# Performance work log

Hardware: AMD Instinct MI355X
Metric: run time of the kernel (lower is better)

## Reference

```python
import jax, jax.numpy as jnp
import numpy as np

H = 16  # attention heads


def setup_inputs() -> dict:
    key = jax.random.key(0)
    k0, k1, k2 = jax.random.split(key, 3)
    B, T, C = 2, 2048, 1024
    x = jax.random.normal(k0, (B, T, C), dtype=jnp.float32)
    W_attn = jax.random.normal(k1, (3 * C, C), dtype=jnp.float32) * 0.02
    W_proj = jax.random.normal(k2, (C, C), dtype=jnp.float32) * 0.02
    b_proj = jnp.zeros((C,), dtype=jnp.float32)
    return {"x": x, "W_attn": W_attn, "W_proj": W_proj, "b_proj": b_proj}


def reference(x, W_attn, W_proj, b_proj):
    # Eval-mode (dropout = identity), rotational_embeddings=False, flash=False path.
    B, T, C = x.shape
    d = C // H
    qkv = jnp.einsum('btc,fc->btf', x, W_attn)          # [B,T,3C] fused QKV proj
    q, k, v = jnp.split(qkv, 3, axis=-1)
    # [B,T,C] -> [B,H,T,d]
    q = q.reshape(B, T, H, d).transpose(0, 2, 1, 3)
    k = k.reshape(B, T, H, d).transpose(0, 2, 1, 3)
    v = v.reshape(B, T, H, d).transpose(0, 2, 1, 3)
    scale = 1.0 / np.sqrt(d).astype(np.float32)
    att = jnp.einsum('bhqd,bhkd->bhqk', q, k) * scale    # full TxT scores (no mask)
    att = jax.nn.softmax(att, axis=-1)
    y = jnp.einsum('bhqk,bhkd->bhqd', att, v)            # [B,H,T,d]
    y = y.transpose(0, 2, 1, 3).reshape(B, T, C)
    return jnp.einsum('btc,oc->bto', y, W_proj) + b_proj
```

## Files before the change

kernel.cpp:

```cpp
#include <hip/hip_runtime.h>
#include <hip/hip_bf16.h>
#include <stdint.h>

typedef __attribute__((ext_vector_type(8))) short bf16x8;
typedef __attribute__((ext_vector_type(4))) float f32x4;
typedef __attribute__((ext_vector_type(4))) unsigned u32x4;

#define MFMA16(A,B,C) __builtin_amdgcn_mfma_f32_16x16x32_bf16(A,B,C,0,0,0)


__device__ inline void gld_lds16(const __hip_bfloat16* g, __hip_bfloat16* l) {
  __builtin_amdgcn_global_load_lds(
      (const __attribute__((address_space(1))) void*)g,
      (__attribute__((address_space(3))) void*)l, 16, 0, 0);
}

__device__ inline unsigned pkbf(float a, float b) {
  __hip_bfloat162 t = __float22bfloat162_rn(float2{a, b});
  return *(unsigned*)&t;
}

__device__ inline void quad_mix(unsigned &a, unsigned &b) {
#if __has_builtin(__builtin_amdgcn_permlane32_swap) && __has_builtin(__builtin_amdgcn_permlane16_swap)
  auto r1 = __builtin_amdgcn_permlane32_swap(a, b, false, false);
  auto r2 = __builtin_amdgcn_permlane16_swap(r1[0], r1[1], false, false);
  a = r2[0];
  b = r2[1];
#else
  int lane = (int)(threadIdx.x & 63);
  int g = lane >> 4;
  int lm = lane & 15;
  int slo = (((g << 1) & 3) << 4) | lm;
  int shi = ((((g << 1) | 1) & 3) << 4) | lm;
  unsigned t0 = (unsigned)__shfl((int)a, slo, 64);
  unsigned t1 = (unsigned)__shfl((int)b, slo, 64);
  unsigned t2 = (unsigned)__shfl((int)a, shi, 64);
  unsigned t3 = (unsigned)__shfl((int)b, shi, 64);
  bool hi = g >= 2;
  unsigned na = hi ? t1 : t0;
  unsigned nb = hi ? t3 : t2;
  a = na;
  b = nb;
#endif
}

__global__ __launch_bounds__(256)
void cvt_bf16(const float* __restrict__ s0, __hip_bfloat16* __restrict__ d0, int n0,
              const float* __restrict__ s1, __hip_bfloat16* __restrict__ d1, int n1,
              const float* __restrict__ s2, __hip_bfloat16* __restrict__ d2, int n2)
{
  const float* s; __hip_bfloat16* d; int n;
  if      (blockIdx.y == 0) { s = s0; d = d0; n = n0; }
  else if (blockIdx.y == 1) { s = s1; d = d1; n = n1; }
  else                      { s = s2; d = d2; n = n2; }
  int idx = (blockIdx.x * 256 + threadIdx.x) * 8;
  if (idx >= n) return;
  float4 u0 = *(const float4*)(s + idx);
  float4 u1 = *(const float4*)(s + idx + 4);
  __hip_bfloat16 t[8];
  t[0] = __float2bfloat16(u0.x); t[1] = __float2bfloat16(u0.y);
  t[2] = __float2bfloat16(u0.z); t[3] = __float2bfloat16(u0.w);
  t[4] = __float2bfloat16(u1.x); t[5] = __float2bfloat16(u1.y);
  t[6] = __float2bfloat16(u1.z); t[7] = __float2bfloat16(u1.w);
  *(int4*)(d + idx) = *(const int4*)t;
}

template<int BM, int BN, typename TC, bool VT, bool FUSE>
__global__ __launch_bounds__(256)
void gemm_bt(const __hip_bfloat16* __restrict__ A,
             const __hip_bfloat16* __restrict__ B,
             TC* __restrict__ C,
             const float* __restrict__ bias,
             __hip_bfloat16* __restrict__ vtg,
             const float* __restrict__ pl,
             int M, int N, int K)
{
  constexpr int MI = BM / 32;
  constexpr int NJ = BN / 32;
  constexpr int NP = (BM + BN) / 64;
  constexpr int SMEM_E = VT ? (((BM + BN) * 32 > 4 * 64 * 72) ? (BM + BN) * 32
                                                              : 4 * 64 * 72)
                            : (BM + BN) * 32;
  __shared__ __align__(16) __hip_bfloat16 smem[SMEM_E];
  __hip_bfloat16* As = smem;
  __hip_bfloat16* Bs = smem + BM * 32;

  const int tid  = threadIdx.x;
  const int lane = tid & 63;
  const int w    = tid >> 6;
  const int lm   = lane & 15;
  const int g    = lane >> 4;

  const int bm = blockIdx.y * BM;
  const int bn = blockIdx.x * BN;
  const int rm = (w >> 1) * (BM / 2);
  const int cn = (w & 1) * (BN / 2);

  const f32x4 fzero = {0.0f, 0.0f, 0.0f, 0.0f};
  f32x4 acc[MI][NJ];
  for (int i = 0; i < MI; i++)
    for (int j = 0; j < NJ; j++)
      acc[i][j] = fzero;

  for (int k0 = 0; k0 < K; k0 += 32) {
    __syncthreads();
#pragma unroll
    for (int p = 0; p < NP; p++) {
      int c = tid + p * 256;
      if (c < BM * 4) {
        if constexpr (FUSE) {
          int row = bm + (c >> 2);
          int col = k0 + (c & 3) * 8;
          int hh  = col >> 6;
          float li = pl[row * 16 + hh] + pl[(size_t)M * 16 + row * 16 + hh];
          float rinv = 1.0f / li;
          int4 ra = *(const int4*)&A[(size_t)row * K + col];
          int4 rb = *(const int4*)&A[(size_t)M * K + (size_t)row * K + col];
          const __hip_bfloat16* pa = (const __hip_bfloat16*)&ra;
          const __hip_bfloat16* pb = (const __hip_bfloat16*)&rb;
          __hip_bfloat16 tt[8];
#pragma unroll
          for (int jj = 0; jj < 8; jj++)
            tt[jj] = __float2bfloat16(
                (__bfloat162float(pa[jj]) + __bfloat162float(pb[jj])) * rinv);
          *(int4*)&As[c * 8] = *(const int4*)tt;
        } else {
          gld_lds16(&A[(size_t)(bm + (c >> 2)) * K + k0 + (c & 3) * 8],
                    &As[c * 8]);
        }
      } else {
        int cb = c - BM * 4;
        gld_lds16(&B[(size_t)(bn + (cb >> 2)) * K + k0 + (cb & 3) * 8], &Bs[cb * 8]);
      }
    }
    __syncthreads();

    bf16x8 af[MI], bfr[NJ];
#pragma unroll
    for (int i = 0; i < MI; i++)
      af[i] = *(const bf16x8*)&As[(rm + 16 * i + lm) * 32 + 8 * g];
#pragma unroll
    for (int j = 0; j < NJ; j++)
      bfr[j] = *(const bf16x8*)&Bs[(cn + 16 * j + lm) * 32 + 8 * g];
#pragma unroll
    for (int i = 0; i < MI; i++)
#pragma unroll
      for (int j = 0; j < NJ; j++)
        acc[i][j] = MFMA16(af[i], bfr[j], acc[i][j]);
  }

  if constexpr (VT) {
    if (vtg != nullptr && bn >= 2048) {
      __syncthreads();
      __hip_bfloat16* scr = smem + w * (64 * 72);
      const int h  = (bn + cn - 2048) >> 6;
      const int bb = bm >> 11;
      const int t0 = (bm & 2047) + rm;
#pragma unroll
      for (int j = 0; j < NJ; j++) {
        int dd = 16 * j + lm;
#pragma unroll
        for (int i = 0; i < MI; i++) {
          __hip_bfloat16 t4[4];
#pragma unroll
          for (int r = 0; r < 4; r++) t4[r] = __float2bfloat16(acc[i][j][r]);
          *(int2*)&scr[dd * 72 + 16 * i + 4 * g] = *(const int2*)t4;
        }
      }
      asm volatile("s_waitcnt lgkmcnt(0)" ::: "memory");
      const int u = lane & 7, ddl = lane >> 3;
#pragma unroll
      for (int it = 0; it < 8; it++) {
        int dd = it * 8 + ddl;
        int4 vrow = *(const int4*)&scr[dd * 72 + u * 8];
        *(int4*)&vtg[((size_t)(bb * 16 + h) * 64 + dd) * 2048 + t0 + u * 8] =
            vrow;
      }
      return;
    }
  }

  const float qs = (VT && vtg != nullptr && bn < 1024)
                       ? (0.125f * 1.4426950408889634f) : 1.0f;
#pragma unroll
  for (int j = 0; j < NJ; j++) {
    int coln = bn + cn + 16 * j + lm;
    float bv = bias ? bias[coln] : 0.0f;
#pragma unroll
    for (int i = 0; i < MI; i++) {
#pragma unroll
      for (int r = 0; r < 4; r++) {
        int rowm = bm + rm + 16 * i + 4 * g + r;
        float v = acc[i][j][r] * qs + bv;
        if constexpr (sizeof(TC) == 2)
          C[(size_t)rowm * N + coln] = __float2bfloat16(v);
        else
          C[(size_t)rowm * N + coln] = v;
      }
    }
  }
}

__global__ __launch_bounds__(256)
void mha(const __hip_bfloat16* __restrict__ qkv,
         const __hip_bfloat16* __restrict__ vtg,
         __hip_bfloat16* __restrict__ yout,
         __hip_bfloat16* __restrict__ po,
         float* __restrict__ pl,
         int nsteps)
{
  const int T = 2048, F = 3072, Cc = 1024;
  const int bh = blockIdx.x;
  const int b  = bh >> 4, h = bh & 15;
  const int qb0 = blockIdx.y * 128;
  const int z   = blockIdx.z;
  const int kvb = z * 64 * nsteps;

  const int tid  = threadIdx.x;
  const int lane = tid & 63;
  const int w    = tid >> 6;
  const int lm   = lane & 15;
  const int g    = lane >> 4;

  __shared__ __align__(16) __hip_bfloat16 Ks[2][64 * 64];
  __shared__ __align__(16) __hip_bfloat16 Vs[2][64 * 64];

  const size_t rowbase = (size_t)b * T * F;
  const int hoff = h * 64;
  const __hip_bfloat16* Kbase = qkv + rowbase + 1024 + hoff;
  const __hip_bfloat16* Vtb   = vtg + (size_t)(b * 16 + h) * 64 * 2048;

  const int qw = qb0 + 32 * w;
  bf16x8 aq[2][2];
#pragma unroll
  for (int mt = 0; mt < 2; mt++)
#pragma unroll
    for (int e = 0; e < 2; e++)
      aq[mt][e] = *(const bf16x8*)
          &qkv[rowbase + (size_t)(qw + 16 * mt + lm) * F + hoff + 32 * e + 8 * g];

  const f32x4 fzero = {0.0f, 0.0f, 0.0f, 0.0f};
  const short one_bf = (short)0x3f80;
  const bf16x8 vone = {one_bf, one_bf, one_bf, one_bf,
                       one_bf, one_bf, one_bf, one_bf};
  f32x4 yacc[2][4];
  f32x4 yl[2];
#pragma unroll
  for (int mt = 0; mt < 2; mt++) {
    yl[mt] = fzero;
#pragma unroll
    for (int c = 0; c < 4; c++) yacc[mt][c] = fzero;
  }

  const int sx = lm & 7;

  auto stage = [&](int tt, int bb) {
    const int kvn = kvb + tt * 64;
#pragma unroll
    for (int p = 0; p < 2; p++) {
      int c = tid + p * 256;
      int row = c >> 3, sl = c & 7, gc = sl ^ (row & 7);
      gld_lds16(Kbase + (size_t)(kvn + row) * F + gc * 8, &Ks[bb][c * 8]);
    }
#pragma unroll
    for (int p = 0; p < 2; p++) {
      int c = tid + p * 256;
      int row = c >> 3, sl = c & 7, gc = sl ^ (row & 7);
      gld_lds16(Vtb + (size_t)row * 2048 + kvn + gc * 8, &Vs[bb][c * 8]);
    }
  };

  stage(0, 0);

  for (int t = 0; t < nsteps; t++) {
    const int buf = t & 1;
    __syncthreads();
    if (t + 1 < nsteps) stage(t + 1, buf ^ 1);

    const __hip_bfloat16* Kb = Ks[buf];
    const __hip_bfloat16* Vb = Vs[buf];

    f32x4 st[2][4];
    __builtin_amdgcn_s_setprio(1);
#pragma unroll
    for (int c2 = 0; c2 < 4; c2++) {
      bf16x8 k0 = *(const bf16x8*)&Kb[(16 * c2 + lm) * 64 + ((0 + g) ^ sx) * 8];
      bf16x8 k1 = *(const bf16x8*)&Kb[(16 * c2 + lm) * 64 + ((4 + g) ^ sx) * 8];
      st[0][c2] = MFMA16(k0, aq[0][0], fzero);
      st[0][c2] = MFMA16(k1, aq[0][1], st[0][c2]);
      st[1][c2] = MFMA16(k0, aq[1][0], fzero);
      st[1][c2] = MFMA16(k1, aq[1][1], st[1][c2]);
    }
    __builtin_amdgcn_s_setprio(0);

    bf16x8 ap[2][2];
#pragma unroll
    for (int mt = 0; mt < 2; mt++) {
#pragma unroll
      for (int hf = 0; hf < 2; hf++) {
        unsigned pkv[2][2];
#pragma unroll
        for (int cc = 0; cc < 2; cc++) {
          const f32x4 &s4 = st[mt][2 * hf + cc];
#pragma unroll
          for (int u = 0; u < 2; u++) {
            float p0 = __builtin_amdgcn_exp2f(s4[2 * u]);
            float p1 = __builtin_amdgcn_exp2f(s4[2 * u + 1]);
            pkv[cc][u] = pkbf(p0, p1);
          }
        }
        unsigned f0 = pkv[0][0], f2 = pkv[1][0];
        quad_mix(f0, f2);
        unsigned f1 = pkv[0][1], f3 = pkv[1][1];
        quad_mix(f1, f3);
        u32x4 fv = {f0, f1, f2, f3};
        ap[mt][hf] = __builtin_bit_cast(bf16x8, fv);
      }
    }

    __builtin_amdgcn_s_setprio(1);
#pragma unroll
    for (int c = 0; c < 4; c++) {
#pragma unroll
      for (int hf = 0; hf < 2; hf++) {
        bf16x8 bv = *(const bf16x8*)
            &Vb[(16 * c + lm) * 64 + (((hf << 2) | g) ^ sx) * 8];
        yacc[0][c] = MFMA16(ap[0][hf], bv, yacc[0][c]);
        yacc[1][c] = MFMA16(ap[1][hf], bv, yacc[1][c]);
      }
    }
#pragma unroll
    for (int mt = 0; mt < 2; mt++) {
      yl[mt] = MFMA16(ap[mt][0], vone, yl[mt]);
      yl[mt] = MFMA16(ap[mt][1], vone, yl[mt]);
    }
    __builtin_amdgcn_s_setprio(0);
  }

#pragma unroll
  for (int mt = 0; mt < 2; mt++) {
    if (yout != nullptr) {
      float rv[4];
#pragma unroll
      for (int r = 0; r < 4; r++)
        rv[r] = 1.0f / yl[mt][r];
#pragma unroll
      for (int c = 0; c < 4; c++)
#pragma unroll
        for (int r = 0; r < 4; r++) {
          int qrow = qw + 16 * mt + 4 * g + r;
          yout[(size_t)(b * T + qrow) * Cc + hoff + 16 * c + lm] =
              __float2bfloat16(yacc[mt][c][r] * rv[r]);
        }
    } else {
      __hip_bfloat16* pz = po + (size_t)z * 4096 * 1024;
      float* plz = pl + (size_t)z * 4096 * 16;
#pragma unroll
      for (int c = 0; c < 4; c++)
#pragma unroll
        for (int r = 0; r < 4; r++) {
          int qrow = qw + 16 * mt + 4 * g + r;
          pz[(size_t)(b * T + qrow) * Cc + hoff + 16 * c + lm] =
              __float2bfloat16(yacc[mt][c][r]);
        }
      if (lm == 0) {
#pragma unroll
        for (int r = 0; r < 4; r++)
          plz[(b * T + qw + 16 * mt + 4 * g + r) * 16 + h] = yl[mt][r];
      }
    }
  }
}

extern "C" void kernel_launch(void* const* d_in, const int* in_sizes, int n_in,
                              void* d_out, int out_size, void* d_ws, size_t ws_size,
                              hipStream_t stream)
{
  const float* x  = (const float*)d_in[0];
  const float* Wa = (const float*)d_in[1];
  const float* Wp = (const float*)d_in[2];
  const float* bp = (const float*)d_in[3];
  float* out = (float*)d_out;

  const int BT = 4096, C = 1024, F3 = 3072;
  char* ws = (char*)d_ws;
  __hip_bfloat16* qkv  = (__hip_bfloat16*)ws;
  __hip_bfloat16* vtg  = (__hip_bfloat16*)(ws + 25165824);
  __hip_bfloat16* xbf  = (__hip_bfloat16*)(ws + 33554432);
  __hip_bfloat16* yb   = xbf;
  __hip_bfloat16* Wabf = (__hip_bfloat16*)(ws + 41943040);
  __hip_bfloat16* Wpbf = (__hip_bfloat16*)(ws + 48234496);
  __hip_bfloat16* Opar = (__hip_bfloat16*)(ws + 50331648);
  float*          lpar = (float*)(ws + 67108864);
  const size_t need_split = 67633152;

  cvt_bf16<<<dim3(2048, 3), 256, 0, stream>>>(
      x, xbf, BT * C, Wa, Wabf, F3 * C, Wp, Wpbf, C * C);
  gemm_bt<128, 128, __hip_bfloat16, true, false>
      <<<dim3(F3 / 128, BT / 128), 256, 0, stream>>>(xbf, Wabf, qkv, nullptr, vtg,
                                                     nullptr, BT, F3, C);
  if (ws_size >= need_split) {
    mha<<<dim3(32, 16, 2), 256, 0, stream>>>(qkv, vtg, nullptr, Opar, lpar, 16);
    gemm_bt<64, 128, float, false, true>
        <<<dim3(C / 128, BT / 64), 256, 0, stream>>>(Opar, Wpbf, out, bp,
                                                     nullptr, lpar, BT, C, C);
  } else {
    mha<<<dim3(32, 16, 1), 256, 0, stream>>>(qkv, vtg, yb, nullptr, nullptr, 32);
    gemm_bt<64, 128, float, false, false>
        <<<dim3(C / 128, BT / 64), 256, 0, stream>>>(yb, Wpbf, out, bp,
                                                     nullptr, nullptr, BT, C, C);
  }
}
```

Before: 214.5 us.

## Deepen GEMM K-tile to 64 with XOR-swizzled LDS and grid remap

The bf16 GEMM now stages 64-wide K tiles instead of 32, halving the number of barrier-separated iterations, and stores them in LDS with an XOR swizzle so MFMA fragment reads avoid bank conflicts. Workgroup IDs are remapped across groups of eight, likely to spread neighbouring tiles across XCDs or caches. The V-transpose epilogue drops its LDS staging buffer and writes 8-byte pieces straight to global memory. Costs are doubled LDS per block, which may lower occupancy, and less coalesced V^T stores.

```diff
diff --git a/kernel.cpp b/kernel.cpp
--- a/kernel.cpp
+++ b/kernel.cpp
@@ -75,24 +75,33 @@
              const float* __restrict__ pl,
              int M, int N, int K)
 {
-  constexpr int MI = BM / 32;
-  constexpr int NJ = BN / 32;
-  constexpr int NP = (BM + BN) / 64;
-  constexpr int SMEM_E = VT ? (((BM + BN) * 32 > 4 * 64 * 72) ? (BM + BN) * 32
-                                                              : 4 * 64 * 72)
-                            : (BM + BN) * 32;
-  __shared__ __align__(16) __hip_bfloat16 smem[SMEM_E];
-  __hip_bfloat16* As = smem;
-  __hip_bfloat16* Bs = smem + BM * 32;
+  constexpr int MI  = BM / 32;
+  constexpr int NJ  = BN / 32;
+  constexpr int ACH = BM * 8;
+  constexpr int NP  = (BM + BN) * 8 / 256;
+
+  __shared__ __align__(16) __hip_bfloat16 As[BM * 64];
+  __shared__ __align__(16) __hip_bfloat16 Bs[BN * 64];
 
   const int tid  = threadIdx.x;
   const int lane = tid & 63;
   const int w    = tid >> 6;
   const int lm   = lane & 15;
   const int g    = lane >> 4;
-
-  const int bm = blockIdx.y * BM;
-  const int bn = blockIdx.x * BN;
+  const int sx   = lm & 7;
+
+  int bxs = blockIdx.x, bys = blockIdx.y;
+  {
+    const int nwg = gridDim.x * gridDim.y;
+    if ((nwg & 7) == 0) {
+      int lid = bys * gridDim.x + bxs;
+      int nl = (lid & 7) * (nwg >> 3) + (lid >> 3);
+      bxs = nl % gridDim.x;
+      bys = nl / gridDim.x;
+    }
+  }
+  const int bm = bys * BM;
+  const int bn = bxs * BN;
   const int rm = (w >> 1) * (BM / 2);
   const int cn = (w & 1) * (BN / 2);
 
@@ -102,20 +111,21 @@
     for (int j = 0; j < NJ; j++)
       acc[i][j] = fzero;
 
-  for (int k0 = 0; k0 < K; k0 += 32) {
+  for (int k0 = 0; k0 < K; k0 += 64) {
     __syncthreads();
 #pragma unroll
     for (int p = 0; p < NP; p++) {
       int c = tid + p * 256;
-      if (c < BM * 4) {
+      if (c < ACH) {
+        int row = c >> 3, sl = c & 7, gc = sl ^ (row & 7);
         if constexpr (FUSE) {
-          int row = bm + (c >> 2);
-          int col = k0 + (c & 3) * 8;
-          int hh  = col >> 6;
-          float li = pl[row * 16 + hh] + pl[(size_t)M * 16 + row * 16 + hh];
+          int grow = bm + row;
+          int col  = k0 + gc * 8;
+          int hh   = col >> 6;
+          float li = pl[grow * 16 + hh] + pl[(size_t)M * 16 + grow * 16 + hh];
           float rinv = 1.0f / li;
-          int4 ra = *(const int4*)&A[(size_t)row * K + col];
-          int4 rb = *(const int4*)&A[(size_t)M * K + (size_t)row * K + col];
+          int4 ra = *(const int4*)&A[(size_t)grow * K + col];
+          int4 rb = *(const int4*)&A[(size_t)M * K + (size_t)grow * K + col];
           const __hip_bfloat16* pa = (const __hip_bfloat16*)&ra;
           const __hip_bfloat16* pb = (const __hip_bfloat16*)&rb;
           __hip_bfloat16 tt[8];
@@ -125,56 +135,51 @@
                 (__bfloat162float(pa[jj]) + __bfloat162float(pb[jj])) * rinv);
           *(int4*)&As[c * 8] = *(const int4*)tt;
         } else {
-          gld_lds16(&A[(size_t)(bm + (c >> 2)) * K + k0 + (c & 3) * 8],
-                    &As[c * 8]);
+          gld_lds16(&A[(size_t)(bm + row) * K + k0 + gc * 8], &As[c * 8]);
         }
       } else {
-        int cb = c - BM * 4;
-        gld_lds16(&B[(size_t)(bn + (cb >> 2)) * K + k0 + (cb & 3) * 8], &Bs[cb * 8]);
+        int cb = c - ACH;
+        int row = cb >> 3, sl = cb & 7, gc = sl ^ (row & 7);
+        gld_lds16(&B[(size_t)(bn + row) * K + k0 + gc * 8], &Bs[cb * 8]);
       }
     }
     __syncthreads();
 
-    bf16x8 af[MI], bfr[NJ];
-#pragma unroll
-    for (int i = 0; i < MI; i++)
-      af[i] = *(const bf16x8*)&As[(rm + 16 * i + lm) * 32 + 8 * g];
-#pragma unroll
-    for (int j = 0; j < NJ; j++)
-      bfr[j] = *(const bf16x8*)&Bs[(cn + 16 * j + lm) * 32 + 8 * g];
-#pragma unroll
-    for (int i = 0; i < MI; i++)
+#pragma unroll
+    for (int e = 0; e < 2; e++) {
+      bf16x8 af[MI], bfr[NJ];
+#pragma unroll
+      for (int i = 0; i < MI; i++)
+        af[i] = *(const bf16x8*)
+            &As[(rm + 16 * i + lm) * 64 + ((4 * e + g) ^ sx) * 8];
 #pragma unroll
       for (int j = 0; j < NJ; j++)
-        acc[i][j] = MFMA16(af[i], bfr[j], acc[i][j]);
+        bfr[j] = *(const bf16x8*)
+            &Bs[(cn + 16 * j + lm) * 64 + ((4 * e + g) ^ sx) * 8];
+#pragma unroll
+      for (int i = 0; i < MI; i++)
+#pragma unroll
+        for (int j = 0; j < NJ; j++)
+          acc[i][j] = MFMA16(af[i], bfr[j], acc[i][j]);
+    }
   }
 
   if constexpr (VT) {
     if (vtg != nullptr && bn >= 2048) {
-      __syncthreads();
-      __hip_bfloat16* scr = smem + w * (64 * 72);
-      const int h  = (bn + cn - 2048) >> 6;
-      const int bb = bm >> 11;
-      const int t0 = (bm & 2047) + rm;
 #pragma unroll
       for (int j = 0; j < NJ; j++) {
-        int dd = 16 * j + lm;
+        int colv = bn + cn + 16 * j + lm - 2048;
+        int vh = colv >> 6, dd = colv & 63;
 #pragma unroll
         for (int i = 0; i < MI; i++) {
+          int m0 = bm + rm + 16 * i + 4 * g;
+          int bb = m0 >> 11, t0 = m0 & 2047;
           __hip_bfloat16 t4[4];
 #pragma unroll
           for (int r = 0; r < 4; r++) t4[r] = __float2bfloat16(acc[i][j][r]);
-          *(int2*)&scr[dd * 72 + 16 * i + 4 * g] = *(const int2*)t4;
+          *(int2*)&vtg[((size_t)(bb * 16 + vh) * 64 + dd) * 2048 + t0] =
+              *(const int2*)t4;
         }
-      }
-      asm volatile("s_waitcnt lgkmcnt(0)" ::: "memory");
-      const int u = lane & 7, ddl = lane >> 3;
-#pragma unroll
-      for (int it = 0; it < 8; it++) {
-        int dd = it * 8 + ddl;
-        int4 vrow = *(const int4*)&scr[dd * 72 + u * 8];
-        *(int4*)&vtg[((size_t)(bb * 16 + h) * 64 + dd) * 2048 + t0 + u * 8] =
-            vrow;
       }
       return;
     }
```

After: 203.9 us. 1.05x faster.
